# Kernel optimization log

Measured on AMD Instinct MI355X. Metric: run time of the kernel, lower is better.

The kernel has to match this reference:

```python
import jax, jax.numpy as jnp
import numpy as np

N = 50000      # nodes
E = 800000     # edges (avg degree 16)
IN_DIM = 128
H = 8          # num_heads
D = 16         # out_dim per head


def setup_inputs() -> dict:
    key = jax.random.key(0)
    ks = jax.random.split(key, 10)
    s = 1.0 / np.sqrt(IN_DIM)
    return {
        "h_src": jax.random.normal(ks[0], (N, IN_DIM), jnp.float32),
        "h_dst": jax.random.normal(ks[1], (N, IN_DIM), jnp.float32),
        "src": jax.random.randint(ks[2], (E,), 0, N),
        "dst": jax.random.randint(ks[3], (E,), 0, N),
        "Qw": jax.random.normal(ks[4], (IN_DIM, H * D), jnp.float32) * s,
        "Qb": jnp.zeros((H * D,), jnp.float32),
        "Kw": jax.random.normal(ks[5], (IN_DIM, H * D), jnp.float32) * s,
        "Kb": jnp.zeros((H * D,), jnp.float32),
        "Vw": jax.random.normal(ks[6], (IN_DIM, H * D), jnp.float32) * s,
        "Vb": jnp.zeros((H * D,), jnp.float32),
    }


def reference(h_src, h_dst, src, dst, Qw, Qb, Kw, Kb, Vw, Vb):
    # Node-level projections: [N, H, D]
    Q = (h_dst @ Qw + Qb).reshape(-1, H, D)
    K = (h_src @ Kw + Kb).reshape(-1, H, D)
    V = (h_src @ Vw + Vb).reshape(-1, H, D)
    # Edge-wise dot product per head: [E, H, 1]
    score = jnp.sum(K[src] * Q[dst], axis=-1, keepdims=True)
    # exp of clamped scaled score (note: clamp(-5,5) BEFORE exp, as in scaled_exp)
    score = jnp.exp(jnp.clip(score / jnp.float32(np.sqrt(D)), -5.0, 5.0))
    # Scatter-sum aggregation onto destination nodes
    wV = jax.ops.segment_sum(score * V[src], dst, num_segments=N)  # [N, H, D]
    z = jax.ops.segment_sum(score, dst, num_segments=N)            # [N, H, 1]
    return wV / z
```

## Files before the change

### kernel.cpp

```cpp
#include <hip/hip_runtime.h>
#include <hip/hip_bf16.h>
#include <math.h>

#define N_NODES 50000
#define E_EDGES 800000
#define IN_DIM  128
#define HD      128
#define SQRT_D_INV 0.25f

#define PROJ_BLOCKS ((N_NODES + 63) / 64)
#define HIST_BLOCKS 1024

typedef __attribute__((ext_vector_type(8))) short short8v;
typedef __attribute__((ext_vector_type(4))) float float4v;

__device__ inline unsigned short f2bf(float x) {
    __hip_bfloat16 b = __float2bfloat16(x);
    return *reinterpret_cast<unsigned short*>(&b);
}
__device__ inline float bflo(unsigned int u) { return __uint_as_float(u << 16); }
__device__ inline float bfhi(unsigned int u) { return __uint_as_float(u & 0xffff0000u); }

__global__ __launch_bounds__(256) void wtr_init_kernel(
    const float* __restrict__ Qw, const float* __restrict__ Kw, const float* __restrict__ Vw,
    unsigned short* __restrict__ wt, int* __restrict__ counts8)
{
    int i = blockIdx.x * 256 + threadIdx.x;
    for (int j = i; j <= 8 * N_NODES; j += 392 * 256) counts8[j] = 0;
    if (i < 3 * 16384) {
        int which = i >> 14;
        int r = i & 16383;
        int k = r >> 7, n = r & 127;
        const float* W = (which == 0) ? Qw : (which == 1) ? Kw : Vw;
        wt[((size_t)which << 14) + n * 128 + k] = f2bf(W[r]);
    }
}

__global__ __launch_bounds__(256) void proj_hist_kernel(
    const float* __restrict__ h_src, const float* __restrict__ h_dst,
    const unsigned short* __restrict__ wt,
    const float* __restrict__ Qb, const float* __restrict__ Kb, const float* __restrict__ Vb,
    unsigned short* __restrict__ qkv,
    const int* __restrict__ dst, int* __restrict__ counts8, int* __restrict__ rank)
{
    if (blockIdx.x >= PROJ_BLOCKS) {
        const int hb = blockIdx.x - PROJ_BLOCKS;
        const int c = hb & 7;
        int* cnt = counts8 + c * N_NODES;
        const int tid = hb * 256 + threadIdx.x;
        const int e0 = tid;
        const int e1 = tid + 262144;
        const int e2 = tid + 524288;
        const int e3 = tid + 786432;
        const bool v3 = (e3 < E_EDGES);
        int d0 = dst[e0], d1 = dst[e1], d2 = dst[e2];
        int d3 = v3 ? dst[e3] : 0;
        int r0 = atomicAdd(&cnt[d0], 1);
        int r1 = atomicAdd(&cnt[d1], 1);
        int r2 = atomicAdd(&cnt[d2], 1);
        int r3 = v3 ? atomicAdd(&cnt[d3], 1) : 0;
        rank[e0] = r0; rank[e1] = r1; rank[e2] = r2;
        if (v3) rank[e3] = r3;
        return;
    }

    __shared__ __align__(16) unsigned short smem[16384];
    const int t  = threadIdx.x;
    const int wv = t >> 6;
    const int l  = t & 63;
    const int lr = l & 15;
    const int kg = l >> 4;
    const int m_base = blockIdx.x * 64 + wv * 16;
    const int arow = min(m_base + lr, N_NODES - 1);

    const float* pd = h_dst + (size_t)arow * IN_DIM;
    const float* ps = h_src + (size_t)arow * IN_DIM;

    short8v afd[4], afs[4];
    #pragma unroll
    for (int ks = 0; ks < 4; ++ks) {
        const int k0 = ks * 32 + kg * 8;
        float4 a0 = *(const float4*)&pd[k0];
        float4 a1 = *(const float4*)&pd[k0 + 4];
        float4 b0 = *(const float4*)&ps[k0];
        float4 b1 = *(const float4*)&ps[k0 + 4];
        afd[ks][0] = (short)f2bf(a0.x); afd[ks][1] = (short)f2bf(a0.y);
        afd[ks][2] = (short)f2bf(a0.z); afd[ks][3] = (short)f2bf(a0.w);
        afd[ks][4] = (short)f2bf(a1.x); afd[ks][5] = (short)f2bf(a1.y);
        afd[ks][6] = (short)f2bf(a1.z); afd[ks][7] = (short)f2bf(a1.w);
        afs[ks][0] = (short)f2bf(b0.x); afs[ks][1] = (short)f2bf(b0.y);
        afs[ks][2] = (short)f2bf(b0.z); afs[ks][3] = (short)f2bf(b0.w);
        afs[ks][4] = (short)f2bf(b1.x); afs[ks][5] = (short)f2bf(b1.y);
        afs[ks][6] = (short)f2bf(b1.z); afs[ks][7] = (short)f2bf(b1.w);
    }

    unsigned short* stg = &smem[wv * 4224];

    #pragma unroll
    for (int phase = 0; phase < 3; ++phase) {
        if (phase) __syncthreads();
        const unsigned short* wsrc = wt + ((size_t)phase << 14);
        #pragma unroll
        for (int j = 0; j < 8; ++j) {
            const int selem = j * 2048 + t * 8;
            const int d = selem * 2;
            const int sd = d ^ (((d >> 8) & 7) << 4);
            *(short8v*)((char*)smem + sd) = *(const short8v*)&wsrc[selem];
        }
        __syncthreads();

        const short8v* aF = (phase == 0) ? afd : afs;
        float4v acc[8];
        #pragma unroll
        for (int i = 0; i < 8; ++i) acc[i] = (float4v)0.f;
        #pragma unroll
        for (int ks = 0; ks < 4; ++ks) {
            #pragma unroll
            for (int nf = 0; nf < 8; ++nf) {
                const int a = (nf * 16 + lr) * 256 + ks * 64 + kg * 16;
                const int sa = a ^ ((lr & 7) << 4);
                short8v bf = *(const short8v*)((const char*)smem + sa);
                acc[nf] = __builtin_amdgcn_mfma_f32_16x16x32_bf16(aF[ks], bf, acc[nf], 0, 0, 0);
            }
        }
        __syncthreads();

        const float* bias = (phase == 0) ? Qb : (phase == 1) ? Kb : Vb;
        #pragma unroll
        for (int nf = 0; nf < 8; ++nf) {
            const float b = bias[nf * 16 + lr];
            #pragma unroll
            for (int r = 0; r < 4; ++r)
                stg[(kg * 4 + r) * 136 + nf * 16 + lr] = f2bf(acc[nf][r] + b);
        }
        #pragma unroll
        for (int i = 0; i < 4; ++i) {
            const int chunk = i * 64 + l;
            const int row = chunk >> 4;
            const int c   = (chunk & 15) * 8;
            const int m = m_base + row;
            short8v v = *(const short8v*)&stg[row * 136 + c];
            if (m < N_NODES) *(short8v*)&qkv[(size_t)m * 384 + phase * 128 + c] = v;
        }
    }
}

__global__ __launch_bounds__(256) void offsets_kernel(const int* __restrict__ counts8,
                                                      int* __restrict__ begc,
                                                      int* __restrict__ begn,
                                                      int* __restrict__ cntn,
                                                      int* __restrict__ total) {
    int n = blockIdx.x * blockDim.x + threadIdx.x;
    int lane = threadIdx.x & 63;
    int pre[8];
    int s = 0;
    if (n < N_NODES) {
        #pragma unroll
        for (int c = 0; c < 8; ++c) {
            int v = counts8[c * N_NODES + n];
            pre[c] = s; s += v;
        }
    }
    int incl = s;
    #pragma unroll
    for (int off = 1; off < 64; off <<= 1) {
        int y = __shfl_up(incl, off);
        if (lane >= off) incl += y;
    }
    int wsum = __shfl(incl, 63);
    int base = 0;
    if (lane == 0) base = atomicAdd(total, wsum);
    base = __shfl(base, 0);
    int b = base + incl - s;
    if (n < N_NODES) {
        begn[n] = b; cntn[n] = s;
        #pragma unroll
        for (int c = 0; c < 8; ++c) begc[c * N_NODES + n] = b + pre[c];
    }
}

__global__ void scatter_kernel(const int* __restrict__ src, const int* __restrict__ dst,
                               const int* __restrict__ begc, const int* __restrict__ rank,
                               int* __restrict__ esrc) {
    int e = blockIdx.x * blockDim.x + threadIdx.x;
    if (e < E_EDGES) {
        int c = (e >> 8) & 7;
        esrc[begc[c * N_NODES + dst[e]] + rank[e]] = src[e];
    }
}

__global__ __launch_bounds__(256) void agg_kernel(
    const unsigned short* __restrict__ qkv,
    const int* __restrict__ begp, const int* __restrict__ cntp,
    const int* __restrict__ esrc, float* __restrict__ out)
{
    int wave = (blockIdx.x * blockDim.x + threadIdx.x) >> 6;
    const int lane = threadIdx.x & 63;
    if (wave >= N_NODES) return;
    const int n = __builtin_amdgcn_readfirstlane(wave);
    const int e = lane >> 4;
    const int u = lane & 15;

    const uint4 qv = *(const uint4*)&qkv[(size_t)n * 384 + u * 8];
    const float q0 = bflo(qv.x), q1 = bfhi(qv.x), q2 = bflo(qv.y), q3 = bfhi(qv.y);
    const float q4 = bflo(qv.z), q5 = bfhi(qv.z), q6 = bflo(qv.w), q7 = bfhi(qv.w);

    const int b0 = begp[n], c0 = cntp[n], endp = b0 + c0;

    float a0=0.f,a1=0.f,a2=0.f,a3=0.f,a4=0.f,a5=0.f,a6=0.f,a7=0.f, z=0.f;

    for (int base = b0; base < endp; base += 16) {
        int idx[4];
        uint4 kk[4], vv[4];
        #pragma unroll
        for (int j = 0; j < 4; ++j) {
            idx[j] = base + j * 4 + e;
            const int s = esrc[min(idx[j], endp - 1)];
            const size_t ro = (size_t)s * 384;
            kk[j] = *(const uint4*)&qkv[ro + 128 + u * 8];
            vv[j] = *(const uint4*)&qkv[ro + 256 + u * 8];
        }
        #pragma unroll
        for (int j = 0; j < 4; ++j) {
            float d =      q0 * bflo(kk[j].x);
            d = fmaf(q1, bfhi(kk[j].x), d);
            d = fmaf(q2, bflo(kk[j].y), d);
            d = fmaf(q3, bfhi(kk[j].y), d);
            d = fmaf(q4, bflo(kk[j].z), d);
            d = fmaf(q5, bfhi(kk[j].z), d);
            d = fmaf(q6, bflo(kk[j].w), d);
            d = fmaf(q7, bfhi(kk[j].w), d);
            d += __shfl_xor(d, 1);
            float w = (idx[j] < endp) ? __expf(fminf(fmaxf(d * SQRT_D_INV, -5.f), 5.f)) : 0.f;
            z += w;
            a0 = fmaf(w, bflo(vv[j].x), a0);
            a1 = fmaf(w, bfhi(vv[j].x), a1);
            a2 = fmaf(w, bflo(vv[j].y), a2);
            a3 = fmaf(w, bfhi(vv[j].y), a3);
            a4 = fmaf(w, bflo(vv[j].z), a4);
            a5 = fmaf(w, bfhi(vv[j].z), a5);
            a6 = fmaf(w, bflo(vv[j].w), a6);
            a7 = fmaf(w, bfhi(vv[j].w), a7);
        }
    }

    #pragma unroll
    for (int mask = 16; mask <= 32; mask <<= 1) {
        z  += __shfl_xor(z, mask);
        a0 += __shfl_xor(a0, mask);
        a1 += __shfl_xor(a1, mask);
        a2 += __shfl_xor(a2, mask);
        a3 += __shfl_xor(a3, mask);
        a4 += __shfl_xor(a4, mask);
        a5 += __shfl_xor(a5, mask);
        a6 += __shfl_xor(a6, mask);
        a7 += __shfl_xor(a7, mask);
    }

    const float inv = 1.f / z;
    if (e == 0) {
        *(float4*)&out[(size_t)n * HD + u * 8]     = make_float4(a0*inv, a1*inv, a2*inv, a3*inv);
        *(float4*)&out[(size_t)n * HD + u * 8 + 4] = make_float4(a4*inv, a5*inv, a6*inv, a7*inv);
    }
}

extern "C" void kernel_launch(void* const* d_in, const int* in_sizes, int n_in,
                              void* d_out, int out_size, void* d_ws, size_t ws_size,
                              hipStream_t stream) {
    const float* h_src = (const float*)d_in[0];
    const float* h_dst = (const float*)d_in[1];
    const int*   src   = (const int*)d_in[2];
    const int*   dst   = (const int*)d_in[3];
    const float* Qw    = (const float*)d_in[4];
    const float* Qb    = (const float*)d_in[5];
    const float* Kw    = (const float*)d_in[6];
    const float* Kb    = (const float*)d_in[7];
    const float* Vw    = (const float*)d_in[8];
    const float* Vb    = (const float*)d_in[9];
    float* out = (float*)d_out;

    char* ws = (char*)d_ws;
    const size_t qkv_bytes = (size_t)N_NODES * 384 * sizeof(unsigned short);
    const size_t wt_bytes  = 3 * 128 * 128 * sizeof(unsigned short);
    unsigned short* qkvp = (unsigned short*)(ws);
    unsigned short* wtp  = (unsigned short*)(ws + qkv_bytes);
    int* counts8 = (int*)(ws + qkv_bytes + wt_bytes);
    int* total   = counts8 + 8 * N_NODES;
    int* begc    = counts8 + 8 * N_NODES + 1;
    int* begn    = begc + 8 * N_NODES;
    int* cntn    = begn + N_NODES;
    int* rank    = cntn + N_NODES;
    int* esrc    = rank + E_EDGES;

    wtr_init_kernel<<<392, 256, 0, stream>>>(Qw, Kw, Vw, wtp, counts8);

    proj_hist_kernel<<<PROJ_BLOCKS + HIST_BLOCKS, 256, 0, stream>>>(
        h_src, h_dst, wtp, Qb, Kb, Vb, qkvp, dst, counts8, rank);

    offsets_kernel<<<(N_NODES + 255) / 256, 256, 0, stream>>>(counts8, begc, begn, cntn, total);

    scatter_kernel<<<(E_EDGES + 255) / 256, 256, 0, stream>>>(src, dst, begc, rank, esrc);

    agg_kernel<<<(N_NODES * 64 + 255) / 256, 256, 0, stream>>>(qkvp, begn, cntn, esrc, out);
}
```

Baseline: 151.6 us.

## Use 512-thread blocks splitting projection N columns across waves, histogram blocks first

The fused projection/histogram kernel moves to 512-thread blocks. The eight waves split each 64-row tile into four row groups by two column halves, which halves per-wave MFMA accumulators and staging size, and one fewer barrier is needed per phase. Histogram blocks are now placed first in the grid and their sub-histogram copy is chosen from contiguous edge ranges (hb>>6), with the scatter kernel's copy index updated to match. The aim is better occupancy and latency hiding, and letting atomics start early. The cost is that weight staging in shared memory is now shared by more waves and total LDS per block grows.

```diff
diff --git a/kernel.cpp b/kernel.cpp
--- a/kernel.cpp
+++ b/kernel.cpp
@@ -8,8 +8,8 @@
 #define HD      128
 #define SQRT_D_INV 0.25f
 
+#define HIST_BLOCKS 512
 #define PROJ_BLOCKS ((N_NODES + 63) / 64)
-#define HIST_BLOCKS 1024
 
 typedef __attribute__((ext_vector_type(8))) short short8v;
 typedef __attribute__((ext_vector_type(4))) float float4v;
@@ -36,41 +36,39 @@
     }
 }
 
-__global__ __launch_bounds__(256) void proj_hist_kernel(
+__global__ __launch_bounds__(512) void proj_hist_kernel(
     const float* __restrict__ h_src, const float* __restrict__ h_dst,
     const unsigned short* __restrict__ wt,
     const float* __restrict__ Qb, const float* __restrict__ Kb, const float* __restrict__ Vb,
     unsigned short* __restrict__ qkv,
     const int* __restrict__ dst, int* __restrict__ counts8, int* __restrict__ rank)
 {
-    if (blockIdx.x >= PROJ_BLOCKS) {
-        const int hb = blockIdx.x - PROJ_BLOCKS;
-        const int c = hb & 7;
+    if (blockIdx.x < HIST_BLOCKS) {
+        const int hb = blockIdx.x;
+        const int c = hb >> 6;
         int* cnt = counts8 + c * N_NODES;
-        const int tid = hb * 256 + threadIdx.x;
-        const int e0 = tid;
-        const int e1 = tid + 262144;
-        const int e2 = tid + 524288;
+        const int tid = hb * 512 + threadIdx.x;
         const int e3 = tid + 786432;
         const bool v3 = (e3 < E_EDGES);
-        int d0 = dst[e0], d1 = dst[e1], d2 = dst[e2];
+        int d0 = dst[tid], d1 = dst[tid + 262144], d2 = dst[tid + 524288];
         int d3 = v3 ? dst[e3] : 0;
         int r0 = atomicAdd(&cnt[d0], 1);
         int r1 = atomicAdd(&cnt[d1], 1);
         int r2 = atomicAdd(&cnt[d2], 1);
-        int r3 = v3 ? atomicAdd(&cnt[d3], 1) : 0;
-        rank[e0] = r0; rank[e1] = r1; rank[e2] = r2;
-        if (v3) rank[e3] = r3;
+        rank[tid] = r0; rank[tid + 262144] = r1; rank[tid + 524288] = r2;
+        if (v3) rank[e3] = atomicAdd(&cnt[d3], 1);
         return;
     }
 
-    __shared__ __align__(16) unsigned short smem[16384];
+    __shared__ __align__(16) unsigned short smem[16384 + 8 * 1152];
     const int t  = threadIdx.x;
-    const int wv = t >> 6;
+    const int w  = t >> 6;
     const int l  = t & 63;
     const int lr = l & 15;
     const int kg = l >> 4;
-    const int m_base = blockIdx.x * 64 + wv * 16;
+    const int wr = w & 3;
+    const int wc = w >> 2;
+    const int m_base = (blockIdx.x - HIST_BLOCKS) * 64 + wr * 16;
     const int arow = min(m_base + lr, N_NODES - 1);
 
     const float* pd = h_dst + (size_t)arow * IN_DIM;
@@ -94,15 +92,14 @@
         afs[ks][6] = (short)f2bf(b1.z); afs[ks][7] = (short)f2bf(b1.w);
     }
 
-    unsigned short* stg = &smem[wv * 4224];
+    unsigned short* stg = &smem[16384 + w * 1152];
 
     #pragma unroll
     for (int phase = 0; phase < 3; ++phase) {
-        if (phase) __syncthreads();
         const unsigned short* wsrc = wt + ((size_t)phase << 14);
         #pragma unroll
-        for (int j = 0; j < 8; ++j) {
-            const int selem = j * 2048 + t * 8;
+        for (int j = 0; j < 4; ++j) {
+            const int selem = j * 4096 + t * 8;
             const int d = selem * 2;
             const int sd = d ^ (((d >> 8) & 7) << 4);
             *(short8v*)((char*)smem + sd) = *(const short8v*)&wsrc[selem];
@@ -110,38 +107,40 @@
         __syncthreads();
 
         const short8v* aF = (phase == 0) ? afd : afs;
-        float4v acc[8];
-        #pragma unroll
-        for (int i = 0; i < 8; ++i) acc[i] = (float4v)0.f;
+        float4v acc[4];
+        #pragma unroll
+        for (int i = 0; i < 4; ++i) acc[i] = (float4v)0.f;
         #pragma unroll
         for (int ks = 0; ks < 4; ++ks) {
             #pragma unroll
-            for (int nf = 0; nf < 8; ++nf) {
-                const int a = (nf * 16 + lr) * 256 + ks * 64 + kg * 16;
+            for (int nf = 0; nf < 4; ++nf) {
+                const int nfg = wc * 4 + nf;
+                const int a = (nfg * 16 + lr) * 256 + ks * 64 + kg * 16;
                 const int sa = a ^ ((lr & 7) << 4);
                 short8v bf = *(const short8v*)((const char*)smem + sa);
                 acc[nf] = __builtin_amdgcn_mfma_f32_16x16x32_bf16(aF[ks], bf, acc[nf], 0, 0, 0);
             }
         }
-        __syncthreads();
 
         const float* bias = (phase == 0) ? Qb : (phase == 1) ? Kb : Vb;
         #pragma unroll
-        for (int nf = 0; nf < 8; ++nf) {
-            const float b = bias[nf * 16 + lr];
+        for (int nf = 0; nf < 4; ++nf) {
+            const float b = bias[wc * 64 + nf * 16 + lr];
             #pragma unroll
             for (int r = 0; r < 4; ++r)
-                stg[(kg * 4 + r) * 136 + nf * 16 + lr] = f2bf(acc[nf][r] + b);
-        }
-        #pragma unroll
-        for (int i = 0; i < 4; ++i) {
+                stg[(kg * 4 + r) * 72 + nf * 16 + lr] = f2bf(acc[nf][r] + b);
+        }
+        #pragma unroll
+        for (int i = 0; i < 2; ++i) {
             const int chunk = i * 64 + l;
-            const int row = chunk >> 4;
-            const int c   = (chunk & 15) * 8;
+            const int row = chunk >> 3;
+            const int cc  = (chunk & 7) * 8;
             const int m = m_base + row;
-            short8v v = *(const short8v*)&stg[row * 136 + c];
-            if (m < N_NODES) *(short8v*)&qkv[(size_t)m * 384 + phase * 128 + c] = v;
-        }
+            short8v v = *(const short8v*)&stg[row * 72 + cc];
+            if (m < N_NODES)
+                *(short8v*)&qkv[(size_t)m * 384 + phase * 128 + wc * 64 + cc] = v;
+        }
+        __syncthreads();
     }
 }
 
@@ -184,7 +183,7 @@
                                int* __restrict__ esrc) {
     int e = blockIdx.x * blockDim.x + threadIdx.x;
     if (e < E_EDGES) {
-        int c = (e >> 8) & 7;
+        int c = (e & 262143) >> 15;
         esrc[begc[c * N_NODES + dst[e]] + rank[e]] = src[e];
     }
 }
@@ -294,7 +293,7 @@
 
     wtr_init_kernel<<<392, 256, 0, stream>>>(Qw, Kw, Vw, wtp, counts8);
 
-    proj_hist_kernel<<<PROJ_BLOCKS + HIST_BLOCKS, 256, 0, stream>>>(
+    proj_hist_kernel<<<HIST_BLOCKS + PROJ_BLOCKS, 512, 0, stream>>>(
         h_src, h_dst, wtp, Qb, Kb, Vb, qkvp, dst, counts8, rank);
 
     offsets_kernel<<<(N_NODES + 255) / 256, 256, 0, stream>>>(counts8, begc, begn, cntn, total);
```

Result: no change. 148.8 us (-1.8%).
